# Performance work log

Hardware: AMD Instinct MI355X
Metric: run time of the kernel (lower is better)

The kernel has to match this reference:

```python
import jax, jax.numpy as jnp
import numpy as np
from jax import lax

B, IMG, P, STRIDE, CIN = 4, 256, 8, 8, 1
D, NH, L = 768, 8, 21
GRID = (IMG - P) // STRIDE + 1  # 32
N = GRID * GRID                 # 1024 tokens
HD = D // NH                    # 96
SCALE = float(HD) ** -0.5


def setup_inputs() -> dict:
    key = jax.random.key(0)
    ks = jax.random.split(key, 9)
    s = 0.02
    return {
        "sam": jax.random.normal(ks[0], (B, CIN, IMG, IMG), dtype=jnp.float32),
        "conv_w": jax.random.normal(ks[1], (D, CIN, P, P), dtype=jnp.float32) * s,
        "conv_b": jnp.zeros((D,), dtype=jnp.float32),
        "ln_g": jnp.ones((D,), dtype=jnp.float32),
        "ln_b": jnp.zeros((D,), dtype=jnp.float32),
        "pos": jax.random.normal(ks[2], (N, D), dtype=jnp.float32) * s,
        "q_w": jax.random.normal(ks[3], (L, D, D), dtype=jnp.float32) * s,
        "kv_w": jax.random.normal(ks[4], (L, D, 2 * D), dtype=jnp.float32) * s,
        "proj_w": jax.random.normal(ks[5], (L, D, D), dtype=jnp.float32) * s,
        "proj_b": jnp.zeros((L, D), dtype=jnp.float32),
    }


def _layernorm(x, g, b, eps=1e-5):
    mu = jnp.mean(x, axis=-1, keepdims=True)
    var = jnp.mean(jnp.square(x - mu), axis=-1, keepdims=True)
    return (x - mu) * lax.rsqrt(var + eps) * g + b


def _guidance(x, qw, kvw, pw, pb):
    b, n, c = x.shape
    q = jnp.einsum('bnc,cd->bnd', x, qw).reshape(b, n, NH, HD).transpose(0, 2, 1, 3)
    kv = jnp.einsum('bnc,cd->bnd', x, kvw)
    k = kv[..., :c].reshape(b, n, NH, HD).transpose(0, 2, 1, 3)
    v = kv[..., c:].reshape(b, n, NH, HD).transpose(0, 2, 1, 3)
    attn = jax.nn.softmax(jnp.einsum('bhnd,bhmd->bhnm', q, k) * SCALE, axis=-1)
    o = jnp.einsum('bhnm,bhmd->bhnd', attn, v).transpose(0, 2, 1, 3).reshape(b, n, c)
    o = jnp.einsum('bnc,cd->bnd', o, pw) + pb
    return o + x  # residual (dropouts are identity in eval)


def reference(sam, conv_w, conv_b, ln_g, ln_b, pos, q_w, kv_w, proj_w, proj_b):
    # Patch embed: conv (valid, stride=patch) -> [B,D,32,32] -> tokens -> LN
    y = lax.conv_general_dilated(sam, conv_w, window_strides=(STRIDE, STRIDE),
                                 padding='VALID',
                                 dimension_numbers=('NCHW', 'OIHW', 'NCHW'))
    y = y + conv_b[None, :, None, None]
    y = y.reshape(B, D, N).transpose(0, 2, 1)  # [B,N,D]
    y = _layernorm(y, ln_g, ln_b)
    x0 = y + pos[None]  # pos_embed(arange) broadcast over batch
    # Faithful to source: each block consumes the SAME x0; output is last block's.
    out = x0
    for i in range(L):
        out = _guidance(x0, q_w[i], kv_w[i], proj_w[i], proj_b[i])
    return out
```

## Files before the change

kernel.cpp:

```cpp
#include <hip/hip_runtime.h>
#include <hip/hip_bf16.h>

typedef __attribute__((ext_vector_type(4))) float f32x4;
typedef __attribute__((ext_vector_type(8))) short s16x8;
typedef unsigned short u16;
typedef unsigned int u32;

#define DEV __device__ __forceinline__

DEV u16 f2bf(float f) {
  union { float f; u32 u; } v; v.f = f;
  u32 r = v.u + 0x7fffu + ((v.u >> 16) & 1u);
  return (u16)(r >> 16);
}
DEV float bf2f(u16 h) {
  union { u32 u; float f; } v; v.u = ((u32)h) << 16;
  return v.f;
}

#define MFMA16(a, b, c) __builtin_amdgcn_mfma_f32_16x16x32_bf16((a), (b), (c), 0, 0, 0)
#define GLD16(g, l) __builtin_amdgcn_global_load_lds((const __attribute__((address_space(1))) u32*)(g), (__attribute__((address_space(3))) u32*)(l), 16, 0, 0)

#define QSCALE 0.10206207261596577f

__global__ __launch_bounds__(256) void prep0_k(
    const float* __restrict__ qw, const float* __restrict__ kvw,
    const float* __restrict__ pw, u16* __restrict__ wqkvT, u16* __restrict__ pwT,
    const float* __restrict__ cw, u16* __restrict__ cwb,
    const float* __restrict__ sam, u16* __restrict__ apx) {
  __shared__ float tb[32][33];
  int bid = blockIdx.x;
  int tid = threadIdx.x;
  if (bid < 2304) {
    int ct = bid / 24, kt = (bid % 24) * 32;
    const float* src;
    u16* dst;
    int ncols, tn, dstbase;
    float scale = 1.0f;
    if (ct < 24) {
      src = qw; ncols = 768; tn = ct * 32; dst = wqkvT; dstbase = tn; scale = QSCALE;
    } else if (ct < 72) {
      src = kvw; ncols = 1536; tn = (ct - 24) * 32; dst = wqkvT; dstbase = 768 + tn;
    } else {
      src = pw; ncols = 768; tn = (ct - 72) * 32; dst = pwT; dstbase = tn;
    }
    int tx = tid & 31, ty = tid >> 5;
#pragma unroll
    for (int i = 0; i < 4; i++)
      tb[ty + i * 8][tx] = src[(size_t)(kt + ty + i * 8) * ncols + tn + tx];
    __syncthreads();
#pragma unroll
    for (int i = 0; i < 4; i++)
      dst[(size_t)(dstbase + ty + i * 8) * 768 + kt + tx] = f2bf(tb[tx][ty + i * 8] * scale);
    return;
  }
  if (bid < 2316) {
    int e0 = (bid - 2304) * 4096 + tid * 16;
    int n = e0 >> 6, k0 = e0 & 63;
    int sx = (n & 7) << 3;
    u16 tmp[16];
#pragma unroll
    for (int j = 0; j < 16; j++) tmp[j] = f2bf(cw[e0 + j]);
#pragma unroll
    for (int h = 0; h < 2; h++)
      *(uint4*)&cwb[n * 64 + ((k0 + h * 8) ^ sx)] = *(const uint4*)&tmp[h * 8];
    return;
  }
  int blk = bid - 2316;
  int b = blk >> 5, gi = blk & 31;
  const float* srow = sam + ((size_t)b * 256 + gi * 8) * 256;
  int gj = tid >> 3, c = tid & 7;
#pragma unroll
  for (int r = 0; r < 8; r++) {
    float v = srow[r * 256 + tid];
    apx[((size_t)b * 1024 + gi * 32 + gj) * 64 + r * 8 + c] = f2bf(v);
  }
}

__global__ __launch_bounds__(256) void convln_k(
    const u16* __restrict__ apx, const u16* __restrict__ cwb,
    const float* __restrict__ cb, const float* __restrict__ g,
    const float* __restrict__ bb, const float* __restrict__ pos,
    u16* __restrict__ x0b) {
  __shared__ __align__(16) u16 Bl[768 * 64];
  __shared__ __align__(16) u16 Al[16 * 72];
  __shared__ float red[4][16][2];
  int tid = threadIdx.x, lane = tid & 63, wid = tid >> 6;
  int l15 = lane & 15, l4 = lane >> 4;
  int tok0 = blockIdx.x * 16;
  {
    const u16* gsrc = cwb + wid * 512 + lane * 8;
    u16* ldst = Bl + wid * 512;
#pragma unroll
    for (int it = 0; it < 24; it++)
      GLD16(gsrc + it * 2048, ldst + it * 2048);
  }
  if (tid < 128) {
    int row = tid >> 3, ch = (tid & 7) * 8;
    *(uint4*)&Al[row * 72 + ch] = *(const uint4*)&apx[(size_t)(tok0 + row) * 64 + ch];
  }
  __syncthreads();
  s16x8 af[2];
#pragma unroll
  for (int kc = 0; kc < 2; kc++)
    af[kc] = *(const s16x8*)&Al[l15 * 72 + kc * 32 + l4 * 8];
  f32x4 s[12];
#pragma unroll
  for (int nt = 0; nt < 12; nt++) {
    int row = wid * 192 + nt * 16 + l15;
    int sx = (row & 7) << 3;
    s16x8 b0 = *(const s16x8*)&Bl[row * 64 + ((l4 * 8) ^ sx)];
    s16x8 b1 = *(const s16x8*)&Bl[row * 64 + ((32 + l4 * 8) ^ sx)];
    f32x4 a = {};
    a = MFMA16(af[0], b0, a);
    a = MFMA16(af[1], b1, a);
    s[nt] = a;
  }
  float p1[4] = {0, 0, 0, 0}, p2[4] = {0, 0, 0, 0};
#pragma unroll
  for (int nt = 0; nt < 12; nt++) {
    float cbv = cb[wid * 192 + nt * 16 + l15];
#pragma unroll
    for (int i = 0; i < 4; i++) {
      float y = s[nt][i] + cbv;
      s[nt][i] = y;
      p1[i] += y;
      p2[i] += y * y;
    }
  }
#pragma unroll
  for (int m = 1; m < 16; m <<= 1)
#pragma unroll
    for (int i = 0; i < 4; i++) {
      p1[i] += __shfl_xor(p1[i], m);
      p2[i] += __shfl_xor(p2[i], m);
    }
  if (l15 == 0)
#pragma unroll
    for (int i = 0; i < 4; i++) {
      red[wid][l4 * 4 + i][0] = p1[i];
      red[wid][l4 * 4 + i][1] = p2[i];
    }
  __syncthreads();
  float mu[4], rs[4];
#pragma unroll
  for (int i = 0; i < 4; i++) {
    int row = l4 * 4 + i;
    float S1 = red[0][row][0] + red[1][row][0] + red[2][row][0] + red[3][row][0];
    float S2 = red[0][row][1] + red[1][row][1] + red[2][row][1] + red[3][row][1];
    mu[i] = S1 * (1.0f / 768.0f);
    float var = S2 * (1.0f / 768.0f) - mu[i] * mu[i];
    rs[i] = rsqrtf(var + 1e-5f);
  }
#pragma unroll
  for (int nt = 0; nt < 12; nt++) {
    int col = wid * 192 + nt * 16 + l15;
    float gg = g[col], bbv = bb[col];
#pragma unroll
    for (int i = 0; i < 4; i++) {
      int tok = tok0 + l4 * 4 + i;
      float val = (s[nt][i] - mu[i]) * rs[i] * gg + bbv +
                  pos[(size_t)(tok & 1023) * 768 + col];
      x0b[(size_t)tok * 768 + col] = f2bf(val);
    }
  }
}

template <int EPI>
__global__ __launch_bounds__(256, 2) void gemm128(
    const u16* __restrict__ A, const u16* __restrict__ BT, int M, int N, int K,
    u16* __restrict__ q, u16* __restrict__ kk_, u16* __restrict__ vt,
    const float* __restrict__ pb, const u16* __restrict__ resb,
    float* __restrict__ outp) {
  __shared__ __align__(16) u16 Al[2][128 * 32];
  __shared__ __align__(16) u16 Bl[2][128 * 32];
  int m0 = blockIdx.y * 128, n0 = blockIdx.x * 128;
  int tid = threadIdx.x, lane = tid & 63, wid = tid >> 6;
  int wr = wid >> 1, wc = wid & 1;
  f32x4 acc[4][4] = {};
  int arow = lane >> 2, acol = (lane & 3) * 8;
  const u16* ag = A + (size_t)(m0 + wid * 32 + arow) * K + acol;
  const u16* bg = BT + (size_t)(n0 + wid * 32 + arow) * K + acol;
  int lofs = wid * 32 * 32;
#define STAGE_G(bufi, kk)                              \
  do {                                                 \
    GLD16(ag + (kk), &Al[bufi][lofs]);                 \
    GLD16(ag + (kk) + 16 * K, &Al[bufi][lofs + 512]);  \
    GLD16(bg + (kk), &Bl[bufi][lofs]);                 \
    GLD16(bg + (kk) + 16 * K, &Bl[bufi][lofs + 512]);  \
  } while (0)
  STAGE_G(0, 0);
  int nk = K >> 5;
  int cur = 0;
  for (int t = 0; t < nk; t++) {
    __syncthreads();
    if (t + 1 < nk) STAGE_G(cur ^ 1, (t + 1) * 32);
    s16x8 af[4], bf[4];
#pragma unroll
    for (int m = 0; m < 4; m++)
      af[m] = *(const s16x8*)&Al[cur][(wr * 64 + m * 16 + (lane & 15)) * 32 + (lane >> 4) * 8];
#pragma unroll
    for (int nn = 0; nn < 4; nn++)
      bf[nn] = *(const s16x8*)&Bl[cur][(wc * 64 + nn * 16 + (lane & 15)) * 32 + (lane >> 4) * 8];
#pragma unroll
    for (int m = 0; m < 4; m++)
#pragma unroll
      for (int nn = 0; nn < 4; nn++)
        acc[m][nn] = MFMA16(af[m], bf[nn], acc[m][nn]);
    cur ^= 1;
  }
#undef STAGE_G
#pragma unroll
  for (int m = 0; m < 4; m++) {
    int rbase = m0 + wr * 64 + m * 16 + ((lane >> 4) << 2);
#pragma unroll
    for (int nn = 0; nn < 4; nn++) {
      int col = n0 + wc * 64 + nn * 16 + (lane & 15);
      f32x4 v = acc[m][nn];
      if (EPI == 0) {
        if (col < 1536) {
          int cc = (col < 768) ? col : col - 768;
          int h = cc / 96, hd = cc % 96;
          u16* dst = (col < 768) ? q : kk_;
          int bq = (rbase >> 10) * 8 + h;
#pragma unroll
          for (int i = 0; i < 4; i++) {
            int row = rbase + i;
            dst[((size_t)bq * 1024 + (row & 1023)) * 96 + hd] = f2bf(v[i]);
          }
        } else {
          int cc = col - 1536;
          int h = cc / 96, hd = cc % 96;
          int bq = (rbase >> 10) * 8 + h;
          ushort4 pk;
          pk.x = f2bf(v[0]); pk.y = f2bf(v[1]); pk.z = f2bf(v[2]); pk.w = f2bf(v[3]);
          *(ushort4*)&vt[((size_t)bq * 96 + hd) * 1024 + (rbase & 1023)] = pk;
        }
      } else {
        float add = pb[col];
#pragma unroll
        for (int i = 0; i < 4; i++) {
          size_t idx = (size_t)(rbase + i) * 768 + col;
          outp[idx] = v[i] + add + bf2f(resb[idx]);
        }
      }
    }
  }
}

__global__ __launch_bounds__(256, 2) void attn_k(
    const u16* __restrict__ qg, const u16* __restrict__ kg,
    const u16* __restrict__ vg, u16* __restrict__ o) {
  int newid = ((blockIdx.x & 7) << 6) + (blockIdx.x >> 3);
  int bh = newid >> 4, qb = newid & 15;
  int b = bh >> 3, h = bh & 7;
  int tid = threadIdx.x, lane = tid & 63, wid = tid >> 6;
  int l15 = lane & 15, l4 = lane >> 4;
  int q0 = qb * 64 + wid * 16;
  const u16* qbase = qg + (size_t)bh * 1024 * 96;
  const u16* kbase = kg + (size_t)bh * 1024 * 96;
  const u16* vbase = vg + (size_t)bh * 96 * 1024;
  s16x8 aq[3];
#pragma unroll
  for (int kc = 0; kc < 3; kc++)
    aq[kc] = *(const s16x8*)&qbase[(size_t)(q0 + l15) * 96 + kc * 32 + l4 * 8];
  float mrun[4], lrun[4];
  f32x4 accO[6] = {};
#pragma unroll
  for (int i = 0; i < 4; i++) { mrun[i] = -1e30f; lrun[i] = 0.0f; }
  __shared__ __align__(16) u16 Kl[64][104];
  __shared__ __align__(16) u16 Pl[4][16][72];
  int kkey[3], koff[3];
#pragma unroll
  for (int it = 0; it < 3; it++) {
    int c = it * 256 + tid;
    kkey[it] = c / 12; koff[it] = (c % 12) * 8;
  }
  for (int kt = 0; kt < 16; kt++) {
#pragma unroll
    for (int it = 0; it < 3; it++)
      *(uint4*)&Kl[kkey[it]][koff[it]] =
          *(const uint4*)&kbase[(size_t)(kt * 64 + kkey[it]) * 96 + koff[it]];
    __syncthreads();
    s16x8 bv[6][2];
#pragma unroll
    for (int nf = 0; nf < 6; nf++)
#pragma unroll
      for (int kc = 0; kc < 2; kc++)
        bv[nf][kc] = *(const s16x8*)&vbase[(size_t)(nf * 16 + l15) * 1024 +
                                           kt * 64 + kc * 32 + l4 * 8];
    f32x4 s4[4] = {};
    __builtin_amdgcn_s_setprio(1);
#pragma unroll
    for (int nf = 0; nf < 4; nf++)
#pragma unroll
      for (int kc = 0; kc < 3; kc++) {
        s16x8 bk = *(const s16x8*)&Kl[nf * 16 + l15][kc * 32 + l4 * 8];
        s4[nf] = MFMA16(aq[kc], bk, s4[nf]);
      }
    __builtin_amdgcn_s_setprio(0);
    float rm[4];
#pragma unroll
    for (int i = 0; i < 4; i++) {
      rm[i] = fmaxf(fmaxf(s4[0][i], s4[1][i]), fmaxf(s4[2][i], s4[3][i]));
#pragma unroll
      for (int m = 1; m < 16; m <<= 1) rm[i] = fmaxf(rm[i], __shfl_xor(rm[i], m));
    }
    bool need = (rm[0] > mrun[0]) || (rm[1] > mrun[1]) ||
                (rm[2] > mrun[2]) || (rm[3] > mrun[3]);
    if (__any(need)) {
#pragma unroll
      for (int i = 0; i < 4; i++) {
        float newm = fmaxf(mrun[i], rm[i]);
        float al = __expf(mrun[i] - newm);
        mrun[i] = newm;
        lrun[i] *= al;
#pragma unroll
        for (int nf = 0; nf < 6; nf++) accO[nf][i] *= al;
      }
    }
#pragma unroll
    for (int i = 0; i < 4; i++) {
      float ps = 0.0f;
#pragma unroll
      for (int nf = 0; nf < 4; nf++) {
        float p = __expf(s4[nf][i] - mrun[i]);
        s4[nf][i] = p;
        ps += p;
      }
#pragma unroll
      for (int m = 1; m < 16; m <<= 1) ps += __shfl_xor(ps, m);
      lrun[i] += ps;
    }
#pragma unroll
    for (int nf = 0; nf < 4; nf++)
#pragma unroll
      for (int i = 0; i < 4; i++)
        Pl[wid][l4 * 4 + i][nf * 16 + l15] = f2bf(s4[nf][i]);
    asm volatile("s_waitcnt lgkmcnt(0)" ::: "memory");
    __builtin_amdgcn_sched_barrier(0);
    __builtin_amdgcn_s_setprio(1);
#pragma unroll
    for (int kc = 0; kc < 2; kc++) {
      s16x8 ap = *(const s16x8*)&Pl[wid][l15][kc * 32 + l4 * 8];
#pragma unroll
      for (int nf = 0; nf < 6; nf++)
        accO[nf] = MFMA16(ap, bv[nf][kc], accO[nf]);
    }
    __builtin_amdgcn_s_setprio(0);
    __syncthreads();
  }
#pragma unroll
  for (int i = 0; i < 4; i++) {
    float inv = 1.0f / lrun[i];
    int tok = q0 + l4 * 4 + i;
    u16* orow = o + ((size_t)(b * 1024 + tok)) * 768 + h * 96;
#pragma unroll
    for (int nf = 0; nf < 6; nf++)
      orow[nf * 16 + l15] = f2bf(accO[nf][i] * inv);
  }
}

extern "C" void kernel_launch(void* const* d_in, const int* in_sizes, int n_in,
                              void* d_out, int out_size, void* d_ws, size_t ws_size,
                              hipStream_t stream) {
  const float* sam    = (const float*)d_in[0];
  const float* conv_w = (const float*)d_in[1];
  const float* conv_b = (const float*)d_in[2];
  const float* ln_g   = (const float*)d_in[3];
  const float* ln_b   = (const float*)d_in[4];
  const float* pos    = (const float*)d_in[5];
  const float* q_w    = (const float*)d_in[6] + (size_t)20 * 768 * 768;
  const float* kv_w   = (const float*)d_in[7] + (size_t)20 * 768 * 1536;
  const float* proj_w = (const float*)d_in[8] + (size_t)20 * 768 * 768;
  const float* proj_b = (const float*)d_in[9] + (size_t)20 * 768;

  char* ws = (char*)d_ws;
  u16* x0b    = (u16*)ws;   ws += (size_t)4096 * 768 * 2;
  u16* wqkvT  = (u16*)ws;   ws += (size_t)2304 * 768 * 2;
  u16* pwT    = (u16*)ws;   ws += (size_t)768 * 768 * 2;
  u16* cwb    = (u16*)ws;   ws += (size_t)768 * 64 * 2;
  u16* apx    = (u16*)ws;   ws += (size_t)4096 * 64 * 2;
  u16* qs     = (u16*)ws;   ws += (size_t)32 * 1024 * 96 * 2;
  u16* ks     = (u16*)ws;   ws += (size_t)32 * 1024 * 96 * 2;
  u16* vts    = (u16*)ws;   ws += (size_t)32 * 96 * 1024 * 2;
  u16* ob     = (u16*)ws;   ws += (size_t)4096 * 768 * 2;

  prep0_k<<<2444, 256, 0, stream>>>(q_w, kv_w, proj_w, wqkvT, pwT,
                                    conv_w, cwb, sam, apx);
  convln_k<<<256, 256, 0, stream>>>(apx, cwb, conv_b, ln_g, ln_b, pos, x0b);
  dim3 g1(18, 32);
  gemm128<0><<<g1, 256, 0, stream>>>(x0b, wqkvT, 4096, 2304, 768, qs, ks, vts,
                                     nullptr, nullptr, nullptr);
  attn_k<<<512, 256, 0, stream>>>(qs, ks, vts, ob);
  dim3 g2(6, 32);
  gemm128<1><<<g2, 256, 0, stream>>>(ob, pwT, 4096, 768, 768, nullptr, nullptr,
                                     nullptr, proj_b, x0b, (float*)d_out);
}
```

Measured before the change: 296.0 us.

## Split attention key range across two wave groups and merge softmax partials

The attention block grows from 256 to 512 threads. Each group of four waves processes half of the 16 key tiles for the same 64 queries, using its own K tile in LDS. At the end, the first half writes its unnormalized output, running max and running sum into LDS, reusing the K buffer. The second half then merges them with the usual log-sum-exp rescaling and writes the result. The goal is to halve the serial key loop per wave and double the number of resident waves to hide latency. The cost is an extra LDS round-trip for the merge, higher LDS use per block, and block-wide barriers shared by both halves.

```diff
diff --git a/kernel.cpp b/kernel.cpp
--- a/kernel.cpp
+++ b/kernel.cpp
@@ -248,15 +248,16 @@
   }
 }
 
-__global__ __launch_bounds__(256, 2) void attn_k(
+__global__ __launch_bounds__(512, 4) void attn_k(
     const u16* __restrict__ qg, const u16* __restrict__ kg,
     const u16* __restrict__ vg, u16* __restrict__ o) {
   int newid = ((blockIdx.x & 7) << 6) + (blockIdx.x >> 3);
   int bh = newid >> 4, qb = newid & 15;
   int b = bh >> 3, h = bh & 7;
   int tid = threadIdx.x, lane = tid & 63, wid = tid >> 6;
+  int half = wid >> 2, wsub = wid & 3;
   int l15 = lane & 15, l4 = lane >> 4;
-  int q0 = qb * 64 + wid * 16;
+  int q0 = qb * 64 + wsub * 16;
   const u16* qbase = qg + (size_t)bh * 1024 * 96;
   const u16* kbase = kg + (size_t)bh * 1024 * 96;
   const u16* vbase = vg + (size_t)bh * 96 * 1024;
@@ -268,18 +269,20 @@
   f32x4 accO[6] = {};
 #pragma unroll
   for (int i = 0; i < 4; i++) { mrun[i] = -1e30f; lrun[i] = 0.0f; }
-  __shared__ __align__(16) u16 Kl[64][104];
-  __shared__ __align__(16) u16 Pl[4][16][72];
+  __shared__ __align__(16) u16 Kl[2][64][104];
+  __shared__ __align__(16) u16 Pl[8][16][72];
+  int ht = tid & 255;
   int kkey[3], koff[3];
 #pragma unroll
   for (int it = 0; it < 3; it++) {
-    int c = it * 256 + tid;
+    int c = it * 256 + ht;
     kkey[it] = c / 12; koff[it] = (c % 12) * 8;
   }
-  for (int kt = 0; kt < 16; kt++) {
+  for (int t = 0; t < 8; t++) {
+    int kt = half * 8 + t;
 #pragma unroll
     for (int it = 0; it < 3; it++)
-      *(uint4*)&Kl[kkey[it]][koff[it]] =
+      *(uint4*)&Kl[half][kkey[it]][koff[it]] =
           *(const uint4*)&kbase[(size_t)(kt * 64 + kkey[it]) * 96 + koff[it]];
     __syncthreads();
     s16x8 bv[6][2];
@@ -295,7 +298,7 @@
     for (int nf = 0; nf < 4; nf++)
 #pragma unroll
       for (int kc = 0; kc < 3; kc++) {
-        s16x8 bk = *(const s16x8*)&Kl[nf * 16 + l15][kc * 32 + l4 * 8];
+        s16x8 bk = *(const s16x8*)&Kl[half][nf * 16 + l15][kc * 32 + l4 * 8];
         s4[nf] = MFMA16(aq[kc], bk, s4[nf]);
       }
     __builtin_amdgcn_s_setprio(0);
@@ -350,14 +353,39 @@
     __builtin_amdgcn_s_setprio(0);
     __syncthreads();
   }
-#pragma unroll
-  for (int i = 0; i < 4; i++) {
-    float inv = 1.0f / lrun[i];
-    int tok = q0 + l4 * 4 + i;
-    u16* orow = o + ((size_t)(b * 1024 + tok)) * 768 + h * 96;
+  float* Cl = (float*)&Kl[0][0][0];
+  float* Ml = Cl + 6400;
+  float* Ll = Ml + 64;
+  if (half == 0) {
 #pragma unroll
     for (int nf = 0; nf < 6; nf++)
-      orow[nf * 16 + l15] = f2bf(accO[nf][i] * inv);
+#pragma unroll
+      for (int i = 0; i < 4; i++)
+        Cl[(wsub * 16 + l4 * 4 + i) * 100 + nf * 16 + l15] = accO[nf][i];
+    if (l15 == 0)
+#pragma unroll
+      for (int i = 0; i < 4; i++) {
+        Ml[wsub * 16 + l4 * 4 + i] = mrun[i];
+        Ll[wsub * 16 + l4 * 4 + i] = lrun[i];
+      }
+  }
+  __syncthreads();
+  if (half == 1) {
+#pragma unroll
+    for (int i = 0; i < 4; i++) {
+      int row = wsub * 16 + l4 * 4 + i;
+      float m0 = Ml[row], l0 = Ll[row];
+      float M = fmaxf(m0, mrun[i]);
+      float e0 = __expf(m0 - M), e1 = __expf(mrun[i] - M);
+      float inv = 1.0f / (l0 * e0 + lrun[i] * e1);
+      int tok = q0 + l4 * 4 + i;
+      u16* orow = o + ((size_t)(b * 1024 + tok)) * 768 + h * 96;
+#pragma unroll
+      for (int nf = 0; nf < 6; nf++) {
+        float v = (Cl[row * 100 + nf * 16 + l15] * e0 + accO[nf][i] * e1) * inv;
+        orow[nf * 16 + l15] = f2bf(v);
+      }
+    }
   }
 }
 
@@ -392,7 +420,7 @@
   dim3 g1(18, 32);
   gemm128<0><<<g1, 256, 0, stream>>>(x0b, wqkvT, 4096, 2304, 768, qs, ks, vts,
                                      nullptr, nullptr, nullptr);
-  attn_k<<<512, 256, 0, stream>>>(qs, ks, vts, ob);
+  attn_k<<<512, 512, 0, stream>>>(qs, ks, vts, ob);
   dim3 g2(6, 32);
   gemm128<1><<<g2, 256, 0, stream>>>(ob, pwT, 4096, 768, 768, nullptr, nullptr,
                                      nullptr, proj_b, x0b, (float*)d_out);
```

After: 305.9 us. 1.03x slower.
